# Optimization experiments

Measured on AMD Instinct MI355X. Metric: run time of the kernel, lower is better.

Reference implementation:

```python
import jax, jax.numpy as jnp
import numpy as np

B, D, LEAVES, MID = 131072, 256, 4, 2


def setup_inputs() -> dict:
    key = jax.random.key(0)
    ks = jax.random.split(key, 5)
    s = 1.0 / np.sqrt(D).astype(np.float32)
    return {
        "x": jax.random.normal(ks[0], (B, D), jnp.float32),
        "Wg": jax.random.normal(ks[1], (D, LEAVES), jnp.float32) * s,
        "bg": jnp.zeros((LEAVES,), jnp.float32),
        "W_leaf": jax.random.normal(ks[2], (LEAVES, D, D), jnp.float32) * s,
        "b_leaf": jnp.zeros((LEAVES, D), jnp.float32),
        "W_mid": jax.random.normal(ks[3], (MID, D, D), jnp.float32) * s,
        "b_mid": jnp.zeros((MID, D), jnp.float32),
        "W_root": jax.random.normal(ks[4], (D, D), jnp.float32) * s,
        "b_root": jnp.zeros((D,), jnp.float32),
    }


def reference(x, Wg, bg, W_leaf, b_leaf, W_mid, b_mid, W_root, b_root):
    # Gate: argmax over leaf experts (torch.max(...).indices over dim=1)
    logits = x @ Wg + bg                      # [B, LEAVES]
    idx = jnp.argmax(logits, axis=1)          # [B] leaf expert per sample
    pidx = idx // 2                           # [B] parent (mid-level) node on the path

    # Leaf level: compute all 4 leaf experts (small E), select routed one.
    h1_all = jax.nn.relu(jnp.einsum('bd,edh->beh', x, W_leaf) + b_leaf)   # [B,4,D]
    h1 = jnp.take_along_axis(h1_all, idx[:, None, None], axis=1)[:, 0]    # [B,D]

    # Mid level: the parent of the selected leaf.
    h2_all = jax.nn.relu(jnp.einsum('bd,pdh->bph', h1, W_mid) + b_mid)    # [B,2,D]
    h2 = jnp.take_along_axis(h2_all, pidx[:, None, None], axis=1)[:, 0]   # [B,D]

    # Root (shared by all paths). end is None -> returned directly.
    return jax.nn.relu(h2 @ W_root + b_root)                              # [B,D]
```

## Files before the change

kernel.cpp:

```cpp
#include <hip/hip_runtime.h>
#include <hip/hip_bf16.h>
#include <stdint.h>

#define B_ROWS 131072
#define DDIM 256
#define GATE_BLOCKS 2048
#define PREPACK_BLOCKS 56
#define MLP_BLOCKS 2051

typedef short bf16x8 __attribute__((ext_vector_type(8)));
typedef float f32x4 __attribute__((ext_vector_type(4)));

__device__ __forceinline__ unsigned short f32_to_bf16_rne(float f) {
    union { float f; uint32_t u; } v; v.f = f;
    uint32_t u = v.u;
    u += 0x7fffu + ((u >> 16) & 1u);
    return (unsigned short)(u >> 16);
}

__device__ __forceinline__ uint32_t cvt_pk_bf16(float a, float b) {
    uint32_t r;
    asm("v_cvt_pk_bf16_f32 %0, %1, %2" : "=v"(r) : "v"(a), "v"(b));
    return r;
}

__global__ __launch_bounds__(256) void gate_prepack_kernel(
    const float* __restrict__ x, const float* __restrict__ Wg,
    const float* __restrict__ bg, const float* __restrict__ Wl,
    const float* __restrict__ Wm, const float* __restrict__ Wr,
    int* __restrict__ counts, int* __restrict__ perm,
    unsigned short* __restrict__ wpack)
{
    __shared__ float smemf[4160];
    int t = threadIdx.x;

    if (blockIdx.x >= GATE_BLOCKS) {
        int bid = blockIdx.x - GATE_BLOCKS;
        int m = bid >> 3, s = bid & 7;
        const float* src = (m < 4) ? (Wl + m * 65536)
                         : (m < 6) ? (Wm + (m - 4) * 65536)
                                   : Wr;
        unsigned short* lds = (unsigned short*)smemf;
        #pragma unroll
        for (int i = 0; i < 8; i++) {
            int v = i * 256 + t;
            int kp = v >> 6;
            int n0 = (v & 63) * 4;
            float4 w = *(const float4*)(src + (32 * s + kp) * 256 + n0);
            #pragma unroll
            for (int c = 0; c < 4; c++) {
                int n = n0 + c;
                float val = (c == 0) ? w.x : (c == 1) ? w.y : (c == 2) ? w.z : w.w;
                int o = (n >> 4) * 512 + ((n & 15) + 16 * (kp >> 3)) * 8 + (kp & 7);
                lds[o] = f32_to_bf16_rne(val);
            }
        }
        __syncthreads();
        uint4* outv = (uint4*)(wpack + (m * 8 + s) * 8192);
        const uint4* ldsv = (const uint4*)lds;
        #pragma unroll
        for (int q = 0; q < 4; q++)
            outv[q * 256 + t] = ldsv[q * 256 + t];
        return;
    }

    float* wgl = smemf;
    int* hcount = (int*)(smemf + 1024);
    int* hbase  = (int*)(smemf + 1028);

    ((float4*)wgl)[t] = ((const float4*)Wg)[t];
    if (t < 4) hcount[t] = 0;
    __syncthreads();

    int lrow = t >> 2, sub = t & 3;
    int row = blockIdx.x * 64 + lrow;
    const float* xr = x + (long)row * DDIM;

    double a0 = 0.0, a1 = 0.0, a2 = 0.0, a3 = 0.0;
    #pragma unroll
    for (int i = 0; i < 16; i++) {
        int k0 = i * 16 + sub * 4;
        float4 v = *(const float4*)(xr + k0);
        #pragma unroll
        for (int kk = 0; kk < 4; kk++) {
            float xv = (kk == 0) ? v.x : (kk == 1) ? v.y : (kk == 2) ? v.z : v.w;
            float4 w = *(const float4*)(wgl + (k0 + kk) * 4);
            a0 += (double)xv * (double)w.x;
            a1 += (double)xv * (double)w.y;
            a2 += (double)xv * (double)w.z;
            a3 += (double)xv * (double)w.w;
        }
    }
    a0 += __shfl_xor(a0, 1); a0 += __shfl_xor(a0, 2);
    a1 += __shfl_xor(a1, 1); a1 += __shfl_xor(a1, 2);
    a2 += __shfl_xor(a2, 1); a2 += __shfl_xor(a2, 2);
    a3 += __shfl_xor(a3, 1); a3 += __shfl_xor(a3, 2);

    int myidx = 0, mylpos = 0;
    if (sub == 0) {
        double l0 = a0 + (double)bg[0];
        double l1 = a1 + (double)bg[1];
        double l2 = a2 + (double)bg[2];
        double l3 = a3 + (double)bg[3];
        double best = l0; myidx = 0;
        if (l1 > best) { best = l1; myidx = 1; }
        if (l2 > best) { best = l2; myidx = 2; }
        if (l3 > best) { best = l3; myidx = 3; }
        mylpos = atomicAdd(&hcount[myidx], 1);
    }
    __syncthreads();
    if (t < 4) hbase[t] = atomicAdd(&counts[t], hcount[t]);
    __syncthreads();
    if (sub == 0) perm[myidx * B_ROWS + hbase[myidx] + mylpos] = row;
}

__global__ __launch_bounds__(256, 4) void mlp_kernel(
    const float* __restrict__ x, const unsigned short* __restrict__ wpack,
    const float* __restrict__ b_leaf, const float* __restrict__ b_mid,
    const float* __restrict__ b_root, const int* __restrict__ counts,
    const int* __restrict__ perm, float* __restrict__ out)
{
    __shared__ unsigned short apack[16384];
    __shared__ int rowsLds[64];

    int c0 = counts[0], c1 = counts[1], c2 = counts[2], c3 = counts[3];
    int t0 = (c0 + 63) >> 6;
    int t01 = t0 + ((c1 + 63) >> 6);
    int t012 = t01 + ((c2 + 63) >> 6);
    int tall = t012 + ((c3 + 63) >> 6);
    int bid = blockIdx.x;
    if (bid >= tall) return;
    int e, tile, cnt;
    if (bid < t0)        { e = 0; tile = bid;        cnt = c0; }
    else if (bid < t01)  { e = 1; tile = bid - t0;   cnt = c1; }
    else if (bid < t012) { e = 2; tile = bid - t01;  cnt = c2; }
    else                 { e = 3; tile = bid - t012; cnt = c3; }
    int base = tile * 64;

    int t = threadIdx.x;
    if (t < 64) {
        int src = base + t;
        rowsLds[t] = perm[e * B_ROWS + (src < cnt ? src : base)];
    }
    __syncthreads();

    {
        int r = t >> 2, sub = t & 3;
        const float* xr = x + (long)rowsLds[r] * DDIM;
        int mt = r >> 4, rl = r & 15;
        #pragma unroll
        for (int i = 0; i < 16; i++) {
            int k0 = i * 16 + sub * 4;
            float4 v = *(const float4*)(xr + k0);
            int s = k0 >> 5;
            int fl = rl + 16 * ((k0 >> 3) & 3);
            uint2 u;
            u.x = cvt_pk_bf16(v.x, v.y);
            u.y = cvt_pk_bf16(v.z, v.w);
            *(uint2*)&apack[((s * 4 + mt) * 64 + fl) * 8 + (k0 & 7)] = u;
        }
    }
    __syncthreads();

    int wv = t >> 6, l = t & 63;
    f32x4 acc[4][4];
    float bias[4];

    auto run_level = [&](const unsigned short* wp, const float* bias_g) {
        #pragma unroll
        for (int nt = 0; nt < 4; nt++)
            bias[nt] = bias_g[(4 * wv + nt) * 16 + (l & 15)];
        f32x4 z = {0.f, 0.f, 0.f, 0.f};
        #pragma unroll
        for (int mt = 0; mt < 4; mt++)
            #pragma unroll
            for (int nt = 0; nt < 4; nt++) acc[mt][nt] = z;

        const bf16x8* wpv = (const bf16x8*)wp;
        #pragma unroll
        for (int s = 0; s < 8; s++) {
            bf16x8 b[4];
            #pragma unroll
            for (int nt = 0; nt < 4; nt++)
                b[nt] = wpv[(s * 16 + 4 * wv + nt) * 64 + l];
            const bf16x8* ap = (const bf16x8*)(apack + s * 4 * 64 * 8);
            #pragma unroll
            for (int mt = 0; mt < 4; mt++) {
                bf16x8 a = ap[mt * 64 + l];
                #pragma unroll
                for (int nt = 0; nt < 4; nt++)
                    acc[mt][nt] = __builtin_amdgcn_mfma_f32_16x16x32_bf16(
                        a, b[nt], acc[mt][nt], 0, 0, 0);
            }
        }
    };

    auto epilogue_lds = [&]() {
        #pragma unroll
        for (int nt = 0; nt < 4; nt++) {
            int col = (4 * wv + nt) * 16 + (l & 15);
            int s = col >> 5;
            int fq = (col >> 3) & 3;
            int j = col & 7;
            int flb = ((l >> 4) << 2) + 16 * fq;
            #pragma unroll
            for (int mt = 0; mt < 4; mt++) {
                float v0 = fmaxf(acc[mt][nt][0] + bias[nt], 0.f);
                float v1 = fmaxf(acc[mt][nt][1] + bias[nt], 0.f);
                float v2 = fmaxf(acc[mt][nt][2] + bias[nt], 0.f);
                float v3 = fmaxf(acc[mt][nt][3] + bias[nt], 0.f);
                uint32_t p01 = cvt_pk_bf16(v0, v1);
                uint32_t p23 = cvt_pk_bf16(v2, v3);
                unsigned short* dst = &apack[((s * 4 + mt) * 64 + flb) * 8 + j];
                dst[0]  = (unsigned short)p01;
                dst[8]  = (unsigned short)(p01 >> 16);
                dst[16] = (unsigned short)p23;
                dst[24] = (unsigned short)(p23 >> 16);
            }
        }
    };

    run_level(wpack + e * 65536, b_leaf + e * 256);
    __syncthreads();
    epilogue_lds();
    __syncthreads();

    run_level(wpack + (4 + (e >> 1)) * 65536, b_mid + (e >> 1) * 256);
    __syncthreads();
    epilogue_lds();
    __syncthreads();

    run_level(wpack + 6 * 65536, b_root);
    #pragma unroll
    for (int nt = 0; nt < 4; nt++) {
        int col = (4 * wv + nt) * 16 + (l & 15);
        #pragma unroll
        for (int mt = 0; mt < 4; mt++) {
            #pragma unroll
            for (int r = 0; r < 4; r++) {
                int row_local = mt * 16 + ((l >> 4) << 2) + r;
                if (base + row_local < cnt) {
                    long grow = rowsLds[row_local];
                    out[grow * DDIM + col] = fmaxf(acc[mt][nt][r] + bias[nt], 0.f);
                }
            }
        }
    }
}

extern "C" void kernel_launch(void* const* d_in, const int* in_sizes, int n_in,
                              void* d_out, int out_size, void* d_ws, size_t ws_size,
                              hipStream_t stream) {
    const float* x      = (const float*)d_in[0];
    const float* Wg     = (const float*)d_in[1];
    const float* bg     = (const float*)d_in[2];
    const float* W_leaf = (const float*)d_in[3];
    const float* b_leaf = (const float*)d_in[4];
    const float* W_mid  = (const float*)d_in[5];
    const float* b_mid  = (const float*)d_in[6];
    const float* W_root = (const float*)d_in[7];
    const float* b_root = (const float*)d_in[8];
    float* out = (float*)d_out;

    char* ws = (char*)d_ws;
    int* counts = (int*)ws;
    int* perm = (int*)(ws + 256);
    unsigned short* wpack = (unsigned short*)(ws + (4 << 20));

    hipMemsetAsync(counts, 0, 16, stream);
    gate_prepack_kernel<<<GATE_BLOCKS + PREPACK_BLOCKS, 256, 0, stream>>>(
        x, Wg, bg, W_leaf, W_mid, W_root, counts, perm, wpack);
    mlp_kernel<<<MLP_BLOCKS, 256, 0, stream>>>(
        x, wpack, b_leaf, b_mid, b_root, counts, perm, out);
}
```

Before: 349.1 us.

## Swap MFMA operands to compute transposed tiles with 512-thread blocks

The MLP kernel now runs 8 waves per block instead of 4, and each wave owns 2 output-column tiles across all 4 row tiles. The MFMA operands are swapped (weights as A, activations as B), so each lane holds 4 consecutive output columns for one row. That allows float4 bias loads, packed uint2 LDS writes in the epilogue, and float4 global stores in place of scalar scattered stores. The trade-off is more waves sharing the same LDS tile, with half the accumulators per wave and a higher occupancy target.

Measured after the change: 334.8 us. 4.1% less time.

```diff
diff --git a/kernel.cpp b/kernel.cpp
--- a/kernel.cpp
+++ b/kernel.cpp
@@ -114,7 +114,7 @@
     if (sub == 0) perm[myidx * B_ROWS + hbase[myidx] + mylpos] = row;
 }
 
-__global__ __launch_bounds__(256, 4) void mlp_kernel(
+__global__ __launch_bounds__(512, 6) void mlp_kernel(
     const float* __restrict__ x, const unsigned short* __restrict__ wpack,
     const float* __restrict__ b_leaf, const float* __restrict__ b_mid,
     const float* __restrict__ b_root, const int* __restrict__ counts,
@@ -145,104 +145,100 @@
     __syncthreads();
 
     {
-        int r = t >> 2, sub = t & 3;
+        int r = t >> 3, sub = t & 7;
         const float* xr = x + (long)rowsLds[r] * DDIM;
-        int mt = r >> 4, rl = r & 15;
-        #pragma unroll
-        for (int i = 0; i < 16; i++) {
-            int k0 = i * 16 + sub * 4;
+        int st = r >> 4, rl = r & 15;
+        #pragma unroll
+        for (int i = 0; i < 8; i++) {
+            int k0 = i * 32 + sub * 4;
             float4 v = *(const float4*)(xr + k0);
             int s = k0 >> 5;
             int fl = rl + 16 * ((k0 >> 3) & 3);
             uint2 u;
             u.x = cvt_pk_bf16(v.x, v.y);
             u.y = cvt_pk_bf16(v.z, v.w);
-            *(uint2*)&apack[((s * 4 + mt) * 64 + fl) * 8 + (k0 & 7)] = u;
+            *(uint2*)&apack[((s * 4 + st) * 64 + fl) * 8 + (k0 & 7)] = u;
         }
     }
     __syncthreads();
 
     int wv = t >> 6, l = t & 63;
-    f32x4 acc[4][4];
-    float bias[4];
-
-    auto run_level = [&](const unsigned short* wp, const float* bias_g) {
-        #pragma unroll
-        for (int nt = 0; nt < 4; nt++)
-            bias[nt] = bias_g[(4 * wv + nt) * 16 + (l & 15)];
+    int q = l >> 4;
+    f32x4 acc[2][4];
+
+    auto run_level = [&](const unsigned short* wp) {
         f32x4 z = {0.f, 0.f, 0.f, 0.f};
         #pragma unroll
-        for (int mt = 0; mt < 4; mt++)
-            #pragma unroll
-            for (int nt = 0; nt < 4; nt++) acc[mt][nt] = z;
+        for (int ot = 0; ot < 2; ot++)
+            #pragma unroll
+            for (int st = 0; st < 4; st++) acc[ot][st] = z;
 
         const bf16x8* wpv = (const bf16x8*)wp;
         #pragma unroll
         for (int s = 0; s < 8; s++) {
-            bf16x8 b[4];
-            #pragma unroll
-            for (int nt = 0; nt < 4; nt++)
-                b[nt] = wpv[(s * 16 + 4 * wv + nt) * 64 + l];
+            bf16x8 wa[2];
+            #pragma unroll
+            for (int ot = 0; ot < 2; ot++)
+                wa[ot] = wpv[(s * 16 + 2 * wv + ot) * 64 + l];
             const bf16x8* ap = (const bf16x8*)(apack + s * 4 * 64 * 8);
             #pragma unroll
-            for (int mt = 0; mt < 4; mt++) {
-                bf16x8 a = ap[mt * 64 + l];
+            for (int st = 0; st < 4; st++) {
+                bf16x8 xb = ap[st * 64 + l];
                 #pragma unroll
-                for (int nt = 0; nt < 4; nt++)
-                    acc[mt][nt] = __builtin_amdgcn_mfma_f32_16x16x32_bf16(
-                        a, b[nt], acc[mt][nt], 0, 0, 0);
+                for (int ot = 0; ot < 2; ot++)
+                    acc[ot][st] = __builtin_amdgcn_mfma_f32_16x16x32_bf16(
+                        wa[ot], xb, acc[ot][st], 0, 0, 0);
             }
         }
     };
 
-    auto epilogue_lds = [&]() {
-        #pragma unroll
-        for (int nt = 0; nt < 4; nt++) {
-            int col = (4 * wv + nt) * 16 + (l & 15);
-            int s = col >> 5;
-            int fq = (col >> 3) & 3;
-            int j = col & 7;
-            int flb = ((l >> 4) << 2) + 16 * fq;
-            #pragma unroll
-            for (int mt = 0; mt < 4; mt++) {
-                float v0 = fmaxf(acc[mt][nt][0] + bias[nt], 0.f);
-                float v1 = fmaxf(acc[mt][nt][1] + bias[nt], 0.f);
-                float v2 = fmaxf(acc[mt][nt][2] + bias[nt], 0.f);
-                float v3 = fmaxf(acc[mt][nt][3] + bias[nt], 0.f);
-                uint32_t p01 = cvt_pk_bf16(v0, v1);
-                uint32_t p23 = cvt_pk_bf16(v2, v3);
-                unsigned short* dst = &apack[((s * 4 + mt) * 64 + flb) * 8 + j];
-                dst[0]  = (unsigned short)p01;
-                dst[8]  = (unsigned short)(p01 >> 16);
-                dst[16] = (unsigned short)p23;
-                dst[24] = (unsigned short)(p23 >> 16);
+    auto epilogue_lds = [&](const float* bias_g) {
+        #pragma unroll
+        for (int ot = 0; ot < 2; ot++) {
+            int kb = (2 * wv + ot) * 16 + 4 * q;
+            float4 bv = *(const float4*)(bias_g + kb);
+            int s2 = kb >> 5;
+            int hq = (kb >> 3) & 3;
+            int jb = kb & 7;
+            #pragma unroll
+            for (int st = 0; st < 4; st++) {
+                float v0 = fmaxf(acc[ot][st][0] + bv.x, 0.f);
+                float v1 = fmaxf(acc[ot][st][1] + bv.y, 0.f);
+                float v2 = fmaxf(acc[ot][st][2] + bv.z, 0.f);
+                float v3 = fmaxf(acc[ot][st][3] + bv.w, 0.f);
+                uint2 u;
+                u.x = cvt_pk_bf16(v0, v1);
+                u.y = cvt_pk_bf16(v2, v3);
+                *(uint2*)&apack[((s2 * 4 + st) * 64 + (l & 15) + 16 * hq) * 8 + jb] = u;
             }
         }
     };
 
-    run_level(wpack + e * 65536, b_leaf + e * 256);
-    __syncthreads();
-    epilogue_lds();
-    __syncthreads();
-
-    run_level(wpack + (4 + (e >> 1)) * 65536, b_mid + (e >> 1) * 256);
-    __syncthreads();
-    epilogue_lds();
-    __syncthreads();
-
-    run_level(wpack + 6 * 65536, b_root);
+    run_level(wpack + e * 65536);
+    __syncthreads();
+    epilogue_lds(b_leaf + e * 256);
+    __syncthreads();
+
+    run_level(wpack + (4 + (e >> 1)) * 65536);
+    __syncthreads();
+    epilogue_lds(b_mid + (e >> 1) * 256);
+    __syncthreads();
+
+    run_level(wpack + 6 * 65536);
     #pragma unroll
-    for (int nt = 0; nt < 4; nt++) {
-        int col = (4 * wv + nt) * 16 + (l & 15);
-        #pragma unroll
-        for (int mt = 0; mt < 4; mt++) {
-            #pragma unroll
-            for (int r = 0; r < 4; r++) {
-                int row_local = mt * 16 + ((l >> 4) << 2) + r;
-                if (base + row_local < cnt) {
-                    long grow = rowsLds[row_local];
-                    out[grow * DDIM + col] = fmaxf(acc[mt][nt][r] + bias[nt], 0.f);
-                }
+    for (int ot = 0; ot < 2; ot++) {
+        int kb = (2 * wv + ot) * 16 + 4 * q;
+        float4 bv = *(const float4*)(b_root + kb);
+        #pragma unroll
+        for (int st = 0; st < 4; st++) {
+            int ls = st * 16 + (l & 15);
+            if (base + ls < cnt) {
+                float4 o4;
+                o4.x = fmaxf(acc[ot][st][0] + bv.x, 0.f);
+                o4.y = fmaxf(acc[ot][st][1] + bv.y, 0.f);
+                o4.z = fmaxf(acc[ot][st][2] + bv.z, 0.f);
+                o4.w = fmaxf(acc[ot][st][3] + bv.w, 0.f);
+                *(float4*)(out + (long)rowsLds[ls] * DDIM + kb) = o4;
             }
         }
     }
@@ -270,6 +266,6 @@
     hipMemsetAsync(counts, 0, 16, stream);
     gate_prepack_kernel<<<GATE_BLOCKS + PREPACK_BLOCKS, 256, 0, stream>>>(
         x, Wg, bg, W_leaf, W_mid, W_root, counts, perm, wpack);
-    mlp_kernel<<<MLP_BLOCKS, 256, 0, stream>>>(
+    mlp_kernel<<<MLP_BLOCKS, 512, 0, stream>>>(
         x, wpack, b_leaf, b_mid, b_root, counts, perm, out);
 }
```
